# Performance work log

Measured on AMD Instinct MI355X. Metric: run time of the kernel, lower is better.

Reference implementation:

```python
import jax, jax.numpy as jnp
import numpy as np

ATTN_MULT = 8.0
NEG_INF = float('-inf')

N, Q, S, D = 16, 2048, 2048, 64


def setup_inputs() -> dict:
    key = jax.random.key(0)
    kq, kk, kv, kp = jax.random.split(key, 4)
    return {
        "queries_nqd": jax.random.normal(kq, (N, Q, D), dtype=jnp.float32),
        "keys_nsd": jax.random.normal(kk, (N, S, D), dtype=jnp.float32),
        "values_nsv": jax.random.normal(kv, (N, S, D), dtype=jnp.float32),
        "prefix_len_n": jax.random.randint(kp, (N,), 0, S, dtype=jnp.int64 if jax.config.jax_enable_x64 else jnp.int32),
    }


def reference(queries_nqd, keys_nsd, values_nsv, prefix_len_n):
    # attention_type == 'block_diagonal', backend == 'torch', dropout p == 0
    n, q, d = queries_nqd.shape
    s = keys_nsd.shape[1]
    scale = ATTN_MULT / d
    # prefix-block mask: key position < prefix_len (broadcast over queries)
    block_mask_n1s = (jnp.arange(s)[None, None, :] < prefix_len_n[:, None, None])  # [n,1,s]
    diag_mask_qs = jnp.arange(q)[:, None] == jnp.arange(s)[None, :]                # [q,s]
    mask_nqs = block_mask_n1s | diag_mask_qs[None, :, :]                           # [n,q,s]
    scores_nqs = jnp.einsum('nqd,nsd->nqs', queries_nqd, keys_nsd) * scale
    scores_nqs = jnp.where(mask_nqs, scores_nqs, NEG_INF)
    probs_nqs = jax.nn.softmax(scores_nqs, axis=-1)
    return jnp.einsum('nqs,nsv->nqv', probs_nqs, values_nsv)
```

## Files before the change

### kernel.cpp

```cpp
#include <hip/hip_runtime.h>
#include <hip/hip_bf16.h>
#include <math.h>

#define NH 16
#define QL 2048
#define SL 2048
#define DD 64
#define BQ 128
#define PSTR 72
#define QK_SCALE_LOG2E 0.1803368801111f

typedef __attribute__((ext_vector_type(8))) short short8;
typedef __attribute__((ext_vector_type(4))) float floatx4;
typedef __attribute__((ext_vector_type(4))) unsigned short ushort4v;
typedef __attribute__((ext_vector_type(8))) unsigned short ushort8v;

__device__ __forceinline__ unsigned short f2bf(float x) {
    unsigned u = __float_as_uint(x);
    u += 0x7FFFu + ((u >> 16) & 1u);
    return (unsigned short)(u >> 16);
}
__device__ __forceinline__ unsigned int f2bf2u(float x, float y) {
    __hip_bfloat162 h = __float22bfloat162_rn(make_float2(x, y));
    return *(unsigned int*)&h;
}
__device__ __forceinline__ float bf2f(unsigned short h) {
    return __uint_as_float((unsigned)h << 16);
}

__device__ __forceinline__ void gld16(const unsigned short* g, unsigned short* l) {
    __builtin_amdgcn_global_load_lds(
        (const __attribute__((address_space(1))) unsigned int*)g,
        (__attribute__((address_space(3))) unsigned int*)l, 16, 0, 0);
}

__global__ __launch_bounds__(256) void prep(
    const float* __restrict__ Kf, const float* __restrict__ Vf,
    unsigned short* __restrict__ Kb, unsigned short* __restrict__ Vtb)
{
    if (blockIdx.y == 0) {
        int idx = blockIdx.x * 256 + threadIdx.x;
        float4 v = ((const float4*)Kf)[idx];
        ushort4v h = { f2bf(v.x), f2bf(v.y), f2bf(v.z), f2bf(v.w) };
        *(ushort4v*)(Kb + (size_t)idx * 4) = h;
    } else {
        if (blockIdx.x >= 512) return;
        __shared__ unsigned short sT[64][PSTR];
        int bx = blockIdx.x;
        int n = bx >> 5, stile = bx & 31, s0 = stile * 64;
        int tid = (int)threadIdx.x;
        const float* vb = Vf + ((size_t)n * SL + s0) * DD;
        #pragma unroll
        for (int i = 0; i < 4; ++i) {
            int idx = tid + i * 256;
            int r = idx >> 4, c = (idx & 15) << 2;
            float4 v = *(const float4*)(vb + r * DD + c);
            sT[c + 0][r] = f2bf(v.x);
            sT[c + 1][r] = f2bf(v.y);
            sT[c + 2][r] = f2bf(v.z);
            sT[c + 3][r] = f2bf(v.w);
        }
        __syncthreads();
        int d = tid >> 2, sg = tid & 3;
        unsigned short* out = Vtb + (size_t)n * DD * SL + (size_t)d * SL + s0 + sg * 16;
        ushort8v a, b;
        #pragma unroll
        for (int i = 0; i < 8; ++i) { a[i] = sT[d][sg * 16 + i]; b[i] = sT[d][sg * 16 + 8 + i]; }
        *(ushort8v*)(out) = a;
        *(ushort8v*)(out + 8) = b;
    }
}

__global__ __launch_bounds__(512, 6) void attn_mfma_split(
    const float* __restrict__ Qf, const unsigned short* __restrict__ Kb,
    const unsigned short* __restrict__ Vtb, const int* __restrict__ plen_g,
    unsigned short* __restrict__ Opb, float* __restrict__ Lp, int spl)
{
    __shared__ unsigned short sK[2][64 * 64];
    __shared__ unsigned short sVt[2][64 * 64];
    __shared__ unsigned short sP[8 * 16 * 64];

    const int blk = blockIdx.x;
    const int n  = blk & (NH - 1);
    const int qt = blk >> 4;
    const int q0 = qt * BQ;
    const int sp = blockIdx.y;
    const int sbeg = sp * spl;
    const int plen = plen_g[n];
    const int ntile = spl >> 6;
    const bool hasdiag = (q0 >= sbeg) && (q0 < sbeg + spl);
    if (!((sbeg < plen) || hasdiag)) return;

    const int tid  = (int)threadIdx.x;
    const int wave = tid >> 6, lane = tid & 63, quad = lane >> 4, l16 = lane & 15;

    int rem  = plen - sbeg;
    int base = (rem > 0) ? min((rem + 63) >> 6, ntile) : 0;
    int td0 = -1, td1 = -1;
    if (hasdiag) {
        int d0 = (q0 - sbeg) >> 6;
        if (d0 >= base) td0 = d0;
        if (d0 + 1 >= base) td1 = d0 + 1;
    }
    const int total = base + (td0 >= 0) + (td1 >= 0);

    const int qrow  = wave * 16 + l16;
    const int qglob = q0 + qrow;
    const int pmask = (l16 & 7) * 8;

    short8 bQ0, bQ1;
    {
        const float* qf = Qf + ((size_t)(n * QL + qglob)) * DD + quad * 8;
        float4 a0 = *(const float4*)(qf);
        float4 a1 = *(const float4*)(qf + 4);
        float4 c0 = *(const float4*)(qf + 32);
        float4 c1 = *(const float4*)(qf + 36);
        const float S = QK_SCALE_LOG2E;
        unsigned int u0[4] = {
            f2bf2u(a0.x * S, a0.y * S), f2bf2u(a0.z * S, a0.w * S),
            f2bf2u(a1.x * S, a1.y * S), f2bf2u(a1.z * S, a1.w * S) };
        unsigned int u1[4] = {
            f2bf2u(c0.x * S, c0.y * S), f2bf2u(c0.z * S, c0.w * S),
            f2bf2u(c1.x * S, c1.y * S), f2bf2u(c1.z * S, c1.w * S) };
        bQ0 = *(short8*)u0;
        bQ1 = *(short8*)u1;
    }

    const unsigned short* kh = Kb  + (size_t)n * SL * DD;
    const unsigned short* vh = Vtb + (size_t)n * DD * SL;

    const int rr = wave * 8 + (lane >> 3);
    const int cg = ((lane & 7) ^ (rr & 7)) * 8;

    auto tile_of = [&](int i) -> int {
        if (i < base) return i;
        if (i == base) return (td0 >= 0) ? td0 : td1;
        return td1;
    };

    {
        int t0 = tile_of(0);
        const unsigned short* kg = kh + (size_t)(sbeg + t0 * 64) * DD;
        const unsigned short* vg = vh + (sbeg + t0 * 64);
        gld16(kg + rr * DD + cg, sK[0] + wave * 512);
        gld16(vg + (size_t)rr * SL + cg, sVt[0] + wave * 512);
    }

    floatx4 acc[4];
    #pragma unroll
    for (int dt = 0; dt < 4; ++dt) acc[dt] = (floatx4){0.f, 0.f, 0.f, 0.f};
    float lsum = 0.f;
    unsigned short* pw = sP + qrow * 64;

    for (int i = 0; i < total; ++i) {
        __syncthreads();

        if (i + 1 < total) {
            int tn = tile_of(i + 1);
            const unsigned short* kg = kh + (size_t)(sbeg + tn * 64) * DD;
            const unsigned short* vg = vh + (sbeg + tn * 64);
            gld16(kg + rr * DD + cg, sK[(i + 1) & 1] + wave * 512);
            gld16(vg + (size_t)rr * SL + cg, sVt[(i + 1) & 1] + wave * 512);
        }

        const unsigned short* sk = sK[i & 1];
        const unsigned short* sv = sVt[i & 1];
        const int t  = tile_of(i);
        const int s0 = sbeg + t * 64;

        floatx4 sf[4];
        #pragma unroll
        for (int st2 = 0; st2 < 4; ++st2) sf[st2] = (floatx4){0.f, 0.f, 0.f, 0.f};
        #pragma unroll
        for (int st2 = 0; st2 < 4; ++st2) {
            int krow = st2 * 16 + l16;
            short8 aK0 = *(const short8*)(sk + krow * 64 + (((0 * 4 + quad) ^ (krow & 7)) * 8));
            short8 aK1 = *(const short8*)(sk + krow * 64 + (((1 * 4 + quad) ^ (krow & 7)) * 8));
            sf[st2] = __builtin_amdgcn_mfma_f32_16x16x32_bf16(aK0, bQ0, sf[st2], 0, 0, 0);
            sf[st2] = __builtin_amdgcn_mfma_f32_16x16x32_bf16(aK1, bQ1, sf[st2], 0, 0, 0);
        }

        if (s0 + 64 <= plen) {
            #pragma unroll
            for (int st2 = 0; st2 < 4; ++st2) {
                float p0 = __builtin_amdgcn_exp2f(sf[st2][0]);
                float p1 = __builtin_amdgcn_exp2f(sf[st2][1]);
                float p2 = __builtin_amdgcn_exp2f(sf[st2][2]);
                float p3 = __builtin_amdgcn_exp2f(sf[st2][3]);
                lsum += (p0 + p1) + (p2 + p3);
                uint2 pk = { f2bf2u(p0, p1), f2bf2u(p2, p3) };
                *(uint2*)(pw + ((st2 * 16 + quad * 4) ^ pmask)) = pk;
            }
        } else {
            #pragma unroll
            for (int st2 = 0; st2 < 4; ++st2) {
                float p[4];
                #pragma unroll
                for (int r = 0; r < 4; ++r) {
                    int s = s0 + st2 * 16 + quad * 4 + r;
                    bool valid = (s < plen) || (s == qglob);
                    p[r] = __builtin_amdgcn_exp2f(valid ? sf[st2][r] : -INFINITY);
                    lsum += p[r];
                }
                uint2 pk = { f2bf2u(p[0], p[1]), f2bf2u(p[2], p[3]) };
                *(uint2*)(pw + ((st2 * 16 + quad * 4) ^ pmask)) = pk;
            }
        }

        #pragma unroll
        for (int ks = 0; ks < 2; ++ks) {
            short8 aP = *(const short8*)(pw + ((ks * 32 + quad * 8) ^ pmask));
            #pragma unroll
            for (int dt = 0; dt < 4; ++dt) {
                int vrow = dt * 16 + l16;
                short8 bV = *(const short8*)(sv + vrow * 64 + (((ks * 4 + quad) ^ (vrow & 7)) * 8));
                acc[dt] = __builtin_amdgcn_mfma_f32_16x16x32_bf16(aP, bV, acc[dt], 0, 0, 0);
            }
        }
    }

    lsum += __shfl_xor(lsum, 16, 64);
    lsum += __shfl_xor(lsum, 32, 64);
    if (quad == 0)
        Lp[((size_t)sp * NH + n) * QL + q0 + qrow] = lsum;

    unsigned short* pws = sP + wave * 16 * 64;
    #pragma unroll
    for (int dt = 0; dt < 4; ++dt) {
        int chunk = dt * 2 + (l16 >> 3);
        #pragma unroll
        for (int r = 0; r < 4; ++r) {
            int row = quad * 4 + r;
            int sw = ((chunk ^ (row & 7)) * 8) + (l16 & 7);
            pws[row * 64 + sw] = f2bf(acc[dt][r]);
        }
    }
    const size_t qbase = ((size_t)sp * NH + n) * QL + q0 + wave * 16;
    #pragma unroll
    for (int t = 0; t < 2; ++t) {
        int row = t * 8 + (lane >> 3);
        int chunk = lane & 7;
        int sw = (chunk ^ (row & 7)) * 8;
        ushort8v val = *(const ushort8v*)(pws + row * 64 + sw);
        *(ushort8v*)(Opb + (qbase + row) * DD + chunk * 8) = val;
    }
}

__global__ __launch_bounds__(256) void combine(
    const unsigned short* __restrict__ Opb, const float* __restrict__ Lp,
    const int* __restrict__ plen_g, float* __restrict__ Og, int nsplit, int spl)
{
    int idx = blockIdx.x * 256 + (int)threadIdx.x;
    int d4 = idx & 15;
    int q  = (idx >> 4) & (QL - 1);
    int n  = idx >> 15;
    int plen = plen_g[n];
    int spd = q / spl;
    float4 s = {0.f, 0.f, 0.f, 0.f};
    float l = 0.f;
    for (int sp = 0; sp < nsplit; ++sp) {
        if ((sp * spl < plen) || (sp == spd)) {
            const unsigned short* ob = Opb + (((size_t)sp * NH + n) * QL + q) * DD + d4 * 4;
            ushort4v v = *(const ushort4v*)(ob);
            s.x += bf2f(v[0]); s.y += bf2f(v[1]); s.z += bf2f(v[2]); s.w += bf2f(v[3]);
            l += Lp[((size_t)sp * NH + n) * QL + q];
        }
    }
    float inv = 1.0f / l;
    float4 o = { s.x * inv, s.y * inv, s.z * inv, s.w * inv };
    *(float4*)(Og + ((size_t)n * QL + q) * DD + d4 * 4) = o;
}

extern "C" void kernel_launch(void* const* d_in, const int* in_sizes, int n_in,
                              void* d_out, int out_size, void* d_ws, size_t ws_size,
                              hipStream_t stream) {
    const float* Qf   = (const float*)d_in[0];
    const float* Kf   = (const float*)d_in[1];
    const float* Vf   = (const float*)d_in[2];
    const int*   plen = (const int*)d_in[3];
    float* Og = (float*)d_out;

    char* ws = (char*)d_ws;
    unsigned short* Kb  = (unsigned short*)(ws);
    unsigned short* Vtb = (unsigned short*)(ws + (4u << 20));
    unsigned short* Opb = (unsigned short*)(ws + (8u << 20));

    const size_t op_bytes = (size_t)NH * QL * DD * 2;
    const size_t lp_bytes = (size_t)NH * QL * 4;
    int nsplit = 1;
    if (ws_size >= (8u << 20) + 4 * (op_bytes + lp_bytes)) nsplit = 4;
    else if (ws_size >= (8u << 20) + 2 * (op_bytes + lp_bytes)) nsplit = 2;
    float* Lp = (float*)(ws + (8u << 20) + (size_t)nsplit * op_bytes);
    int spl = SL / nsplit;

    prep<<<dim3(2048, 2), 256, 0, stream>>>(Kf, Vf, Kb, Vtb);
    attn_mfma_split<<<dim3(NH * (QL / BQ), nsplit), 512, 0, stream>>>(Qf, Kb, Vtb, plen, Opb, Lp, spl);
    combine<<<2048, 256, 0, stream>>>(Opb, Lp, plen, Og, nsplit, spl);
}
```

Before: 111.3 us.

## Fix split count at two, merge prep work, add MFMA priority, widen combine

The sequence split is fixed at two compile-time partitions instead of being picked at runtime from workspace size, and the 2D grid is flattened with a rotated head mapping. The prep kernel now handles K conversion and V transpose in one block per tile with 512 threads. The first K/V tile prefetch moves ahead of Q loading, s_setprio brackets the MFMA sections, and combine processes 8 outputs per thread. If the workspace previously allowed four splits, this may lose parallelism, and the fixed layout assumes the workspace is large enough.

```diff
diff --git a/kernel.cpp b/kernel.cpp
--- a/kernel.cpp
+++ b/kernel.cpp
@@ -7,6 +7,9 @@
 #define SL 2048
 #define DD 64
 #define BQ 128
+#define NSPLIT 2
+#define SPL 1024
+#define NTILE 16
 #define PSTR 72
 #define QK_SCALE_LOG2E 0.1803368801111f
 
@@ -34,68 +37,68 @@
         (__attribute__((address_space(3))) unsigned int*)l, 16, 0, 0);
 }
 
-__global__ __launch_bounds__(256) void prep(
+__global__ __launch_bounds__(512) void k_prep(
     const float* __restrict__ Kf, const float* __restrict__ Vf,
     unsigned short* __restrict__ Kb, unsigned short* __restrict__ Vtb)
 {
-    if (blockIdx.y == 0) {
-        int idx = blockIdx.x * 256 + threadIdx.x;
+    __shared__ unsigned short sT[64][PSTR];
+    const int bx = (int)blockIdx.x, tid = (int)threadIdx.x;
+
+    const int gidx = bx * 512 + tid;
+    #pragma unroll
+    for (int k = 0; k < 2; ++k) {
+        int idx = gidx + k * (512 * 512);
         float4 v = ((const float4*)Kf)[idx];
         ushort4v h = { f2bf(v.x), f2bf(v.y), f2bf(v.z), f2bf(v.w) };
         *(ushort4v*)(Kb + (size_t)idx * 4) = h;
-    } else {
-        if (blockIdx.x >= 512) return;
-        __shared__ unsigned short sT[64][PSTR];
-        int bx = blockIdx.x;
-        int n = bx >> 5, stile = bx & 31, s0 = stile * 64;
-        int tid = (int)threadIdx.x;
-        const float* vb = Vf + ((size_t)n * SL + s0) * DD;
-        #pragma unroll
-        for (int i = 0; i < 4; ++i) {
-            int idx = tid + i * 256;
-            int r = idx >> 4, c = (idx & 15) << 2;
-            float4 v = *(const float4*)(vb + r * DD + c);
-            sT[c + 0][r] = f2bf(v.x);
-            sT[c + 1][r] = f2bf(v.y);
-            sT[c + 2][r] = f2bf(v.z);
-            sT[c + 3][r] = f2bf(v.w);
-        }
-        __syncthreads();
-        int d = tid >> 2, sg = tid & 3;
-        unsigned short* out = Vtb + (size_t)n * DD * SL + (size_t)d * SL + s0 + sg * 16;
-        ushort8v a, b;
-        #pragma unroll
-        for (int i = 0; i < 8; ++i) { a[i] = sT[d][sg * 16 + i]; b[i] = sT[d][sg * 16 + 8 + i]; }
-        *(ushort8v*)(out) = a;
-        *(ushort8v*)(out + 8) = b;
-    }
-}
-
-__global__ __launch_bounds__(512, 6) void attn_mfma_split(
+    }
+
+    const int n = bx >> 5, s0 = (bx & 31) * 64;
+    const float* vb = Vf + ((size_t)n * SL + s0) * DD;
+    #pragma unroll
+    for (int i = 0; i < 2; ++i) {
+        int idx = tid + i * 512;
+        int r = idx >> 4, c = (idx & 15) << 2;
+        float4 v = *(const float4*)(vb + r * DD + c);
+        sT[c + 0][r] = f2bf(v.x);
+        sT[c + 1][r] = f2bf(v.y);
+        sT[c + 2][r] = f2bf(v.z);
+        sT[c + 3][r] = f2bf(v.w);
+    }
+    __syncthreads();
+    const int d = tid >> 3, sg = tid & 7;
+    unsigned short* out = Vtb + (size_t)n * DD * SL + (size_t)d * SL + s0 + sg * 8;
+    ushort8v a;
+    #pragma unroll
+    for (int i = 0; i < 8; ++i) a[i] = sT[d][sg * 8 + i];
+    *(ushort8v*)out = a;
+}
+
+__global__ __launch_bounds__(512, 6) void k_attn(
     const float* __restrict__ Qf, const unsigned short* __restrict__ Kb,
     const unsigned short* __restrict__ Vtb, const int* __restrict__ plen_g,
-    unsigned short* __restrict__ Opb, float* __restrict__ Lp, int spl)
+    unsigned short* __restrict__ Opb, float* __restrict__ Lp)
 {
     __shared__ unsigned short sK[2][64 * 64];
     __shared__ unsigned short sVt[2][64 * 64];
     __shared__ unsigned short sP[8 * 16 * 64];
 
-    const int blk = blockIdx.x;
-    const int n  = blk & (NH - 1);
-    const int qt = blk >> 4;
-    const int q0 = qt * BQ;
-    const int sp = blockIdx.y;
-    const int sbeg = sp * spl;
+    const int flat = (int)blockIdx.x;
+    const int sp   = flat >> 8;
+    const int rb   = flat & 255;
+    const int n    = (rb + sp) & (NH - 1);
+    const int qt   = rb >> 4;
+    const int q0   = qt * BQ;
+    const int sbeg = sp * SPL;
     const int plen = plen_g[n];
-    const int ntile = spl >> 6;
-    const bool hasdiag = (q0 >= sbeg) && (q0 < sbeg + spl);
+    const bool hasdiag = (q0 >= sbeg) && (q0 < sbeg + SPL);
     if (!((sbeg < plen) || hasdiag)) return;
 
     const int tid  = (int)threadIdx.x;
     const int wave = tid >> 6, lane = tid & 63, quad = lane >> 4, l16 = lane & 15;
 
     int rem  = plen - sbeg;
-    int base = (rem > 0) ? min((rem + 63) >> 6, ntile) : 0;
+    int base = (rem > 0) ? min((rem + 63) >> 6, NTILE) : 0;
     int td0 = -1, td1 = -1;
     if (hasdiag) {
         int d0 = (q0 - sbeg) >> 6;
@@ -107,6 +110,26 @@
     const int qrow  = wave * 16 + l16;
     const int qglob = q0 + qrow;
     const int pmask = (l16 & 7) * 8;
+
+    const unsigned short* kh = Kb  + (size_t)n * SL * DD;
+    const unsigned short* vh = Vtb + (size_t)n * DD * SL;
+
+    const int srow = wave * 8 + (lane >> 3);
+    const int scol = ((lane & 7) ^ (srow & 7)) * 8;
+
+    auto tile_of = [&](int i) -> int {
+        if (i < base) return i;
+        if (i == base) return (td0 >= 0) ? td0 : td1;
+        return td1;
+    };
+
+    {
+        int t0 = tile_of(0);
+        const unsigned short* kg = kh + (size_t)(sbeg + t0 * 64) * DD;
+        const unsigned short* vg = vh + (sbeg + t0 * 64);
+        gld16(kg + srow * DD + scol, sK[0] + wave * 512);
+        gld16(vg + (size_t)srow * SL + scol, sVt[0] + wave * 512);
+    }
 
     short8 bQ0, bQ1;
     {
@@ -126,26 +149,6 @@
         bQ1 = *(short8*)u1;
     }
 
-    const unsigned short* kh = Kb  + (size_t)n * SL * DD;
-    const unsigned short* vh = Vtb + (size_t)n * DD * SL;
-
-    const int rr = wave * 8 + (lane >> 3);
-    const int cg = ((lane & 7) ^ (rr & 7)) * 8;
-
-    auto tile_of = [&](int i) -> int {
-        if (i < base) return i;
-        if (i == base) return (td0 >= 0) ? td0 : td1;
-        return td1;
-    };
-
-    {
-        int t0 = tile_of(0);
-        const unsigned short* kg = kh + (size_t)(sbeg + t0 * 64) * DD;
-        const unsigned short* vg = vh + (sbeg + t0 * 64);
-        gld16(kg + rr * DD + cg, sK[0] + wave * 512);
-        gld16(vg + (size_t)rr * SL + cg, sVt[0] + wave * 512);
-    }
-
     floatx4 acc[4];
     #pragma unroll
     for (int dt = 0; dt < 4; ++dt) acc[dt] = (floatx4){0.f, 0.f, 0.f, 0.f};
@@ -159,8 +162,8 @@
             int tn = tile_of(i + 1);
             const unsigned short* kg = kh + (size_t)(sbeg + tn * 64) * DD;
             const unsigned short* vg = vh + (sbeg + tn * 64);
-            gld16(kg + rr * DD + cg, sK[(i + 1) & 1] + wave * 512);
-            gld16(vg + (size_t)rr * SL + cg, sVt[(i + 1) & 1] + wave * 512);
+            gld16(kg + srow * DD + scol, sK[(i + 1) & 1] + wave * 512);
+            gld16(vg + (size_t)srow * SL + scol, sVt[(i + 1) & 1] + wave * 512);
         }
 
         const unsigned short* sk = sK[i & 1];
@@ -171,6 +174,7 @@
         floatx4 sf[4];
         #pragma unroll
         for (int st2 = 0; st2 < 4; ++st2) sf[st2] = (floatx4){0.f, 0.f, 0.f, 0.f};
+        __builtin_amdgcn_s_setprio(1);
         #pragma unroll
         for (int st2 = 0; st2 < 4; ++st2) {
             int krow = st2 * 16 + l16;
@@ -179,6 +183,7 @@
             sf[st2] = __builtin_amdgcn_mfma_f32_16x16x32_bf16(aK0, bQ0, sf[st2], 0, 0, 0);
             sf[st2] = __builtin_amdgcn_mfma_f32_16x16x32_bf16(aK1, bQ1, sf[st2], 0, 0, 0);
         }
+        __builtin_amdgcn_s_setprio(0);
 
         if (s0 + 64 <= plen) {
             #pragma unroll
@@ -196,17 +201,18 @@
             for (int st2 = 0; st2 < 4; ++st2) {
                 float p[4];
                 #pragma unroll
-                for (int r = 0; r < 4; ++r) {
-                    int s = s0 + st2 * 16 + quad * 4 + r;
+                for (int r2 = 0; r2 < 4; ++r2) {
+                    int s = s0 + st2 * 16 + quad * 4 + r2;
                     bool valid = (s < plen) || (s == qglob);
-                    p[r] = __builtin_amdgcn_exp2f(valid ? sf[st2][r] : -INFINITY);
-                    lsum += p[r];
+                    p[r2] = __builtin_amdgcn_exp2f(valid ? sf[st2][r2] : -INFINITY);
+                    lsum += p[r2];
                 }
                 uint2 pk = { f2bf2u(p[0], p[1]), f2bf2u(p[2], p[3]) };
                 *(uint2*)(pw + ((st2 * 16 + quad * 4) ^ pmask)) = pk;
             }
         }
 
+        __builtin_amdgcn_s_setprio(1);
         #pragma unroll
         for (int ks = 0; ks < 2; ++ks) {
             short8 aP = *(const short8*)(pw + ((ks * 32 + quad * 8) ^ pmask));
@@ -217,6 +223,7 @@
                 acc[dt] = __builtin_amdgcn_mfma_f32_16x16x32_bf16(aP, bV, acc[dt], 0, 0, 0);
             }
         }
+        __builtin_amdgcn_s_setprio(0);
     }
 
     lsum += __shfl_xor(lsum, 16, 64);
@@ -229,16 +236,16 @@
     for (int dt = 0; dt < 4; ++dt) {
         int chunk = dt * 2 + (l16 >> 3);
         #pragma unroll
-        for (int r = 0; r < 4; ++r) {
-            int row = quad * 4 + r;
+        for (int r2 = 0; r2 < 4; ++r2) {
+            int row = quad * 4 + r2;
             int sw = ((chunk ^ (row & 7)) * 8) + (l16 & 7);
-            pws[row * 64 + sw] = f2bf(acc[dt][r]);
+            pws[row * 64 + sw] = f2bf(acc[dt][r2]);
         }
     }
     const size_t qbase = ((size_t)sp * NH + n) * QL + q0 + wave * 16;
     #pragma unroll
-    for (int t = 0; t < 2; ++t) {
-        int row = t * 8 + (lane >> 3);
+    for (int t2 = 0; t2 < 2; ++t2) {
+        int row = t2 * 8 + (lane >> 3);
         int chunk = lane & 7;
         int sw = (chunk ^ (row & 7)) * 8;
         ushort8v val = *(const ushort8v*)(pws + row * 64 + sw);
@@ -246,29 +253,36 @@
     }
 }
 
-__global__ __launch_bounds__(256) void combine(
+__global__ __launch_bounds__(512) void k_combine(
     const unsigned short* __restrict__ Opb, const float* __restrict__ Lp,
-    const int* __restrict__ plen_g, float* __restrict__ Og, int nsplit, int spl)
+    const int* __restrict__ plen_g, float* __restrict__ Og)
 {
-    int idx = blockIdx.x * 256 + (int)threadIdx.x;
-    int d4 = idx & 15;
-    int q  = (idx >> 4) & (QL - 1);
-    int n  = idx >> 15;
-    int plen = plen_g[n];
-    int spd = q / spl;
-    float4 s = {0.f, 0.f, 0.f, 0.f};
+    const int idx = (int)(blockIdx.x * 512 + threadIdx.x);
+    const int d8 = idx & 7;
+    const int q  = (idx >> 3) & (QL - 1);
+    const int n  = idx >> 14;
+    const int plen = plen_g[n];
+    const int spd = q >> 10;
+    float s[8];
+    #pragma unroll
+    for (int j = 0; j < 8; ++j) s[j] = 0.f;
     float l = 0.f;
-    for (int sp = 0; sp < nsplit; ++sp) {
-        if ((sp * spl < plen) || (sp == spd)) {
-            const unsigned short* ob = Opb + (((size_t)sp * NH + n) * QL + q) * DD + d4 * 4;
-            ushort4v v = *(const ushort4v*)(ob);
-            s.x += bf2f(v[0]); s.y += bf2f(v[1]); s.z += bf2f(v[2]); s.w += bf2f(v[3]);
+    #pragma unroll
+    for (int sp = 0; sp < NSPLIT; ++sp) {
+        if ((sp * SPL < plen) || (sp == spd)) {
+            const unsigned short* ob = Opb + (((size_t)sp * NH + n) * QL + q) * DD + d8 * 8;
+            ushort8v v = *(const ushort8v*)ob;
+            #pragma unroll
+            for (int j = 0; j < 8; ++j) s[j] += bf2f(v[j]);
             l += Lp[((size_t)sp * NH + n) * QL + q];
         }
     }
-    float inv = 1.0f / l;
-    float4 o = { s.x * inv, s.y * inv, s.z * inv, s.w * inv };
-    *(float4*)(Og + ((size_t)n * QL + q) * DD + d4 * 4) = o;
+    const float inv = 1.0f / l;
+    float4 o0 = { s[0] * inv, s[1] * inv, s[2] * inv, s[3] * inv };
+    float4 o1 = { s[4] * inv, s[5] * inv, s[6] * inv, s[7] * inv };
+    float* og = Og + ((size_t)n * QL + q) * DD + d8 * 8;
+    *(float4*)og = o0;
+    *(float4*)(og + 4) = o1;
 }
 
 extern "C" void kernel_launch(void* const* d_in, const int* in_sizes, int n_in,
@@ -284,16 +298,9 @@
     unsigned short* Kb  = (unsigned short*)(ws);
     unsigned short* Vtb = (unsigned short*)(ws + (4u << 20));
     unsigned short* Opb = (unsigned short*)(ws + (8u << 20));
-
-    const size_t op_bytes = (size_t)NH * QL * DD * 2;
-    const size_t lp_bytes = (size_t)NH * QL * 4;
-    int nsplit = 1;
-    if (ws_size >= (8u << 20) + 4 * (op_bytes + lp_bytes)) nsplit = 4;
-    else if (ws_size >= (8u << 20) + 2 * (op_bytes + lp_bytes)) nsplit = 2;
-    float* Lp = (float*)(ws + (8u << 20) + (size_t)nsplit * op_bytes);
-    int spl = SL / nsplit;
-
-    prep<<<dim3(2048, 2), 256, 0, stream>>>(Kf, Vf, Kb, Vtb);
-    attn_mfma_split<<<dim3(NH * (QL / BQ), nsplit), 512, 0, stream>>>(Qf, Kb, Vtb, plen, Opb, Lp, spl);
-    combine<<<2048, 256, 0, stream>>>(Opb, Lp, plen, Og, nsplit, spl);
-}
+    float*          Lp  = (float*)(ws + (16u << 20));
+
+    k_prep<<<512, 512, 0, stream>>>(Kf, Vf, Kb, Vtb);
+    k_attn<<<NSPLIT * 256, 512, 0, stream>>>(Qf, Kb, Vtb, plen, Opb, Lp);
+    k_combine<<<512, 512, 0, stream>>>(Opb, Lp, plen, Og);
+}
```

Measured after the change: 107.2 us. 3.7% less time.
